# Performance work log

Hardware: AMD Instinct MI355X
Metric: run time of the kernel (lower is better)

## Reference

```python
import jax, jax.numpy as jnp
import numpy as np
from jax.ops import segment_sum

N_NODES = 100000
N_EDGES = 3200000
N_GRAPHS = 64


def gcn_conv(x, W, b, src, dst, n_nodes):
    # Linear transform first (PyG GCNConv applies lin before propagate)
    h = x @ W  # [N, out]
    # Add self loops
    loop = jnp.arange(n_nodes, dtype=src.dtype)
    s = jnp.concatenate([src, loop])
    d = jnp.concatenate([dst, loop])
    # Symmetric normalization deg^-1/2 (deg counts incoming edges incl. self loop)
    deg = segment_sum(jnp.ones_like(d, dtype=h.dtype), d, num_segments=n_nodes)
    dinv = jnp.where(deg > 0, jax.lax.rsqrt(deg), 0.0)
    norm = dinv[s] * dinv[d]  # [E+N]
    # Gather messages from source, scale, scatter-add to target
    msg = h[s] * norm[:, None]
    out = segment_sum(msg, d, num_segments=n_nodes)
    return out + b


def setup_inputs() -> dict:
    key = jax.random.key(0)
    ks = jax.random.split(key, 6)
    x = jax.random.normal(ks[0], (N_NODES, 128), dtype=jnp.float32)
    edge_index = jax.random.randint(ks[1], (2, N_EDGES), 0, N_NODES, dtype=jnp.int64)
    batch = jnp.sort(jax.random.randint(ks[2], (N_NODES,), 0, N_GRAPHS, dtype=jnp.int64))
    W1 = jax.random.normal(ks[3], (128, 256), dtype=jnp.float32) * (1.0 / np.sqrt(128))
    b1 = jnp.zeros((256,), dtype=jnp.float32)
    W2 = jax.random.normal(ks[4], (256, 128), dtype=jnp.float32) * (1.0 / np.sqrt(256))
    b2 = jnp.zeros((128,), dtype=jnp.float32)
    return {"x": x, "edge_index": edge_index, "batch": batch,
            "W1": W1, "b1": b1, "W2": W2, "b2": b2, "num_graphs": N_GRAPHS}


def reference(x, edge_index, batch, W1, b1, W2, b2, num_graphs):
    n_nodes = x.shape[0]
    src, dst = edge_index[0], edge_index[1]
    # dropout(p=0.6, training=False) is identity at inference
    h = jax.nn.relu(gcn_conv(x, W1, b1, src, dst, n_nodes))
    h = gcn_conv(h, W2, b2, src, dst, n_nodes)
    # global_mean_pool by graph id
    sums = segment_sum(h, batch, num_segments=num_graphs)
    counts = segment_sum(jnp.ones((n_nodes,), dtype=h.dtype), batch, num_segments=num_graphs)
    return sums / jnp.maximum(counts, 1.0)[:, None]
```

## Files before the change

### kernel.cpp

```cpp
#include <hip/hip_runtime.h>
#include <hip/hip_bf16.h>
#include <stdint.h>

#define N_NODES 100000
#define N_EDGES 3200000
#define N_GRAPHS 64
#define BSH 8
#define NB 391
#define G_SC 512
#define EPB 6250

typedef unsigned int u32;
typedef unsigned short u16;
typedef __attribute__((ext_vector_type(8))) short bf16x8;
typedef __attribute__((ext_vector_type(4))) float f32x4;

__device__ __forceinline__ float bf_lo(u32 u){ return __uint_as_float(u << 16); }
__device__ __forceinline__ float bf_hi(u32 u){ return __uint_as_float(u & 0xffff0000u); }
__device__ __forceinline__ u16 f2bf(float f){
    union { __hip_bfloat16 h; u16 u; } c; c.h = __float2bfloat16(f); return c.u;
}
__device__ __forceinline__ u32 pack2(float a, float b){
    return (u32)f2bf(a) | ((u32)f2bf(b) << 16);
}

__global__ __launch_bounds__(512) void k_hist(const int* __restrict__ dst,
                                              int* __restrict__ hist){
    __shared__ int h[NB];
    int tid = threadIdx.x, g = blockIdx.x;
    for (int i = tid; i < NB; i += 512) h[i] = 0;
    __syncthreads();
    const int2* d2 = reinterpret_cast<const int2*>(dst + g * EPB);
    for (int i = tid; i < EPB / 2; i += 512){
        int2 d = d2[i];
        atomicAdd(&h[d.x >> BSH], 1);
        atomicAdd(&h[d.y >> BSH], 1);
    }
    __syncthreads();
    for (int i = tid; i < NB; i += 512) hist[i * G_SC + g] = h[i];
}

__global__ __launch_bounds__(512) void k_colscan(const int* __restrict__ hist,
                                                 int* __restrict__ cursors,
                                                 int* __restrict__ btot){
    __shared__ int sm[512];
    int b = blockIdx.x, tid = threadIdx.x;
    int v = hist[b * G_SC + tid];
    sm[tid] = v; __syncthreads();
    for (int off = 1; off < 512; off <<= 1){
        int t = (tid >= off) ? sm[tid - off] : 0;
        __syncthreads(); sm[tid] += t; __syncthreads();
    }
    cursors[b * G_SC + tid] = sm[tid] - v;
    if (tid == 511) btot[b] = sm[511];
}

__global__ __launch_bounds__(512) void k_bscan(const int* __restrict__ btot,
                                               int* __restrict__ bbase){
    __shared__ int sm[512];
    int tid = threadIdx.x;
    int v = (tid < NB) ? btot[tid] : 0;
    sm[tid] = v; __syncthreads();
    for (int off = 1; off < 512; off <<= 1){
        int t = (tid >= off) ? sm[tid - off] : 0;
        __syncthreads(); sm[tid] += t; __syncthreads();
    }
    if (tid < NB) bbase[tid] = sm[tid] - v;
    if (tid == 0) bbase[NB] = N_EDGES;
}

__global__ __launch_bounds__(512) void k_scatter(const int* __restrict__ src,
                                                 const int* __restrict__ dst,
                                                 const int* __restrict__ cursors,
                                                 const int* __restrict__ bbase,
                                                 uint2* __restrict__ pairs){
    __shared__ int cur[NB];
    int g = blockIdx.x, tid = threadIdx.x;
    for (int i = tid; i < NB; i += 512) cur[i] = cursors[i * G_SC + g] + bbase[i];
    __syncthreads();
    const int2* s2 = reinterpret_cast<const int2*>(src + g * EPB);
    const int2* d2 = reinterpret_cast<const int2*>(dst + g * EPB);
    for (int i = tid; i < EPB / 2; i += 512){
        int2 s = s2[i]; int2 d = d2[i];
        int p0 = atomicAdd(&cur[d.x >> BSH], 1);
        pairs[p0] = make_uint2((u32)s.x, (u32)d.x);
        int p1 = atomicAdd(&cur[d.y >> BSH], 1);
        pairs[p1] = make_uint2((u32)s.y, (u32)d.y);
    }
}

__global__ __launch_bounds__(512) void k_fine(const uint2* __restrict__ pairs,
                                              const int* __restrict__ bbase,
                                              int* __restrict__ offsets,
                                              float* __restrict__ dinv,
                                              int* __restrict__ csr_src){
    __shared__ int ldeg[256];
    __shared__ int ssc[256];
    __shared__ int lcur[256];
    int b = blockIdx.x, tid = threadIdx.x;
    int node0 = b << BSH;
    if (tid < 256) ldeg[tid] = 0;
    __syncthreads();
    int e0 = bbase[b], e1 = bbase[b + 1];
    for (int e = e0 + tid; e < e1; e += 512)
        atomicAdd(&ldeg[pairs[e].y - node0], 1);
    __syncthreads();
    int myDeg = (tid < 256) ? ldeg[tid] : 0;
    if (tid < 256) ssc[tid] = myDeg;
    __syncthreads();
    for (int off = 1; off < 256; off <<= 1){
        int t = 0;
        if (tid >= off && tid < 256) t = ssc[tid - off];
        __syncthreads();
        if (tid < 256) ssc[tid] += t;
        __syncthreads();
    }
    if (tid < 256){
        int excl = ssc[tid] - myDeg;
        int n = node0 + tid;
        if (n <= N_NODES) offsets[n] = e0 + excl;
        if (n < N_NODES)  dinv[n] = rsqrtf((float)myDeg + 1.0f);
        lcur[tid] = e0 + excl;
    }
    __syncthreads();
    for (int e = e0 + tid; e < e1; e += 512){
        uint2 p = pairs[e];
        int pos = atomicAdd(&lcur[p.y - node0], 1);
        csr_src[pos] = (int)p.x;
    }
}

__global__ void k_cvt_x(const float* __restrict__ x, const float* __restrict__ dinv,
                        u32* __restrict__ xb){
    int i = blockIdx.x * blockDim.x + threadIdx.x;
    if (i < N_NODES * 32){
        float w = dinv[i >> 5];
        float4 f = reinterpret_cast<const float4*>(x)[i];
        uint2 p = make_uint2(pack2(f.x * w, f.y * w), pack2(f.z * w, f.w * w));
        reinterpret_cast<uint2*>(xb)[i] = p;
    }
}

__global__ void k_cvt_w(const float* __restrict__ W1, const float* __restrict__ W2,
                        u16* __restrict__ w1t, u16* __restrict__ w2t){
    int i = blockIdx.x * blockDim.x + threadIdx.x;
    if (i < 128 * 256){
        int n = i / 128, k = i % 128;
        w1t[i] = f2bf(W1[k * 256 + n]);
    } else {
        int j = i - 128 * 256;
        int n = j / 256, k = j % 256;
        w2t[j] = f2bf(W2[k * 128 + n]);
    }
}

template<bool OUT_BF16>
__global__ __launch_bounds__(256) void k_agg(const u32* __restrict__ X,
                      const int* __restrict__ offs, const int* __restrict__ csr_src,
                      const float* __restrict__ dinv, void* __restrict__ out){
    int lane = threadIdx.x & 63;
    int v = blockIdx.x * 4 + (threadIdx.x >> 6);
    u32 u = X[v * 64 + lane];
    float a0 = bf_lo(u), a1 = bf_hi(u);
    int e1 = offs[v + 1];
    for (int e = offs[v]; e < e1; e += 64){
        int idx = e + lane;
        int sv = (idx < e1) ? csr_src[idx] : 0;
        int cnt = min(64, e1 - e);
        int j = 0;
        for (; j + 4 <= cnt; j += 4){
            int s0 = __shfl(sv, j), s1 = __shfl(sv, j+1), s2 = __shfl(sv, j+2), s3 = __shfl(sv, j+3);
            u32 u0 = X[s0*64 + lane], u1 = X[s1*64 + lane], u2 = X[s2*64 + lane], u3 = X[s3*64 + lane];
            a0 += (bf_lo(u0) + bf_lo(u1)) + (bf_lo(u2) + bf_lo(u3));
            a1 += (bf_hi(u0) + bf_hi(u1)) + (bf_hi(u2) + bf_hi(u3));
        }
        for (; j < cnt; j++){
            int s = __shfl(sv, j);
            u32 uu = X[s*64 + lane];
            a0 += bf_lo(uu); a1 += bf_hi(uu);
        }
    }
    float w = dinv[v];
    a0 *= w; a1 *= w;
    if (OUT_BF16){
        ((u32*)out)[v*64 + lane] = pack2(a0, a1);
    } else {
        ((float2*)out)[v*64 + lane] = make_float2(a0, a1);
    }
}

template<int BK, int BN, bool RELU, bool BIAS, bool SCALE>
__global__ __launch_bounds__(256) void k_gemm(const u16* __restrict__ A, const u16* __restrict__ BT,
                        const float* __restrict__ bias, const float* __restrict__ rowscale,
                        u16* __restrict__ C, int M){
    extern __shared__ char smem[];
    char* As = smem;
    char* Bs = smem + 64 * BK * 2;
    const int tid = threadIdx.x;
    const int rowbytes = BK * 2;
    {
        const int a16 = 64 * rowbytes / 16;
        for (int it = tid; it < a16; it += 256){
            int flat = it * 16;
            int r = flat / rowbytes, cb = flat % rowbytes;
            int grow = blockIdx.x * 64 + r;
            int4 val = make_int4(0,0,0,0);
            if (grow < M) val = *reinterpret_cast<const int4*>(A + grow * BK + cb / 2);
            *reinterpret_cast<int4*>(As + r * rowbytes + (cb ^ ((r & 7) << 4))) = val;
        }
        const int b16 = BN * rowbytes / 16;
        for (int it = tid; it < b16; it += 256){
            int flat = it * 16;
            int r = flat / rowbytes, cb = flat % rowbytes;
            int4 val = *reinterpret_cast<const int4*>(BT + r * BK + cb / 2);
            *reinterpret_cast<int4*>(Bs + r * rowbytes + (cb ^ ((r & 7) << 4))) = val;
        }
    }
    __syncthreads();

    const int wid = tid >> 6, lane = tid & 63;
    const int r0 = wid * 16;
    constexpr int NF = BN / 16;
    f32x4 acc[NF];
#pragma unroll
    for (int i = 0; i < NF; i++) acc[i] = (f32x4){0.f,0.f,0.f,0.f};
    const int ar = r0 + (lane & 15);
    const int koff = (lane >> 4) * 8;
#pragma unroll
    for (int kb = 0; kb < BK / 32; kb++){
        int kbyte = (kb * 32 + koff) * 2;
        bf16x8 aF = *reinterpret_cast<const bf16x8*>(As + ar * rowbytes + (kbyte ^ ((ar & 7) << 4)));
#pragma unroll
        for (int nf = 0; nf < NF; nf++){
            int bn = nf * 16 + (lane & 15);
            bf16x8 bF = *reinterpret_cast<const bf16x8*>(Bs + bn * rowbytes + (kbyte ^ ((bn & 7) << 4)));
            acc[nf] = __builtin_amdgcn_mfma_f32_16x16x32_bf16(aF, bF, acc[nf], 0, 0, 0);
        }
    }
#pragma unroll
    for (int nf = 0; nf < NF; nf++){
        int col = nf * 16 + (lane & 15);
        float bv = BIAS ? bias[col] : 0.f;
#pragma unroll
        for (int j = 0; j < 4; j++){
            int grow = blockIdx.x * 64 + r0 + (lane >> 4) * 4 + j;
            if (grow < M){
                float val = acc[nf][j] + bv;
                if (RELU) val = fmaxf(val, 0.f);
                if (SCALE) val *= rowscale[grow];
                C[grow * BN + col] = f2bf(val);
            }
        }
    }
}

__global__ void k_pool(const float* __restrict__ agg2f, const int* __restrict__ batch,
                       float* __restrict__ psum, float* __restrict__ counts){
    const int NPB = 200;
    int n0 = blockIdx.x * NPB, n1 = min(n0 + NPB, N_NODES);
    int tid = threadIdx.x;
    float racc = 0.f; int gcur = batch[n0]; int runlen = 0;
    for (int n = n0; n < n1; n++){
        int g = batch[n];
        if (g != gcur){
            atomicAdd(&psum[gcur * 128 + tid], racc);
            if (tid == 0) atomicAdd(&counts[gcur], (float)runlen);
            racc = 0.f; runlen = 0; gcur = g;
        }
        racc += agg2f[n * 128 + tid];
        runlen++;
    }
    atomicAdd(&psum[gcur * 128 + tid], racc);
    if (tid == 0) atomicAdd(&counts[gcur], (float)runlen);
}

__global__ void k_final(const float* __restrict__ psum, const float* __restrict__ counts,
                        const float* __restrict__ b2, float* __restrict__ out){
    int g = blockIdx.x, c = threadIdx.x;
    out[g * 128 + c] = psum[g * 128 + c] / fmaxf(counts[g], 1.0f) + b2[c];
}

extern "C" void kernel_launch(void* const* d_in, const int* in_sizes, int n_in,
                              void* d_out, int out_size, void* d_ws, size_t ws_size,
                              hipStream_t stream){
    const float* x   = (const float*)d_in[0];
    const int*   ei  = (const int*)d_in[1];
    const int* batch = (const int*)d_in[2];
    const float* W1  = (const float*)d_in[3];
    const float* b1  = (const float*)d_in[4];
    const float* W2  = (const float*)d_in[5];
    const float* b2  = (const float*)d_in[6];
    float* out = (float*)d_out;
    const int* esrc = ei;
    const int* edst = ei + N_EDGES;

    char* w = (char*)d_ws;
    size_t off = 0;
    auto alloc = [&](size_t bytes) -> char* {
        char* p = w + off; off += (bytes + 255) & ~size_t(255); return p;
    };
    float* dinv     = (float*)alloc((size_t)N_NODES * 4);
    int*   offsets  = (int*)  alloc((size_t)(N_NODES + 1) * 4);
    int*   hist     = (int*)  alloc((size_t)NB * G_SC * 4);
    int*   cursors  = (int*)  alloc((size_t)NB * G_SC * 4);
    int*   btot     = (int*)  alloc((size_t)NB * 4);
    int*   bbase    = (int*)  alloc((size_t)(NB + 1) * 4);
    int*   csr_src  = (int*)  alloc((size_t)N_EDGES * 4);
    u32*   xb       = (u32*)  alloc((size_t)N_NODES * 64 * 4);
    u16*   aggx     = (u16*)  alloc((size_t)N_NODES * 128 * 2);
    u16*   h        = (u16*)  alloc((size_t)N_NODES * 256 * 2);
    u16*   t        = (u16*)  alloc((size_t)N_NODES * 128 * 2);
    u16*   w1t      = (u16*)  alloc(128 * 256 * 2);
    u16*   w2t      = (u16*)  alloc(256 * 128 * 2);
    float* psum     = (float*)alloc((size_t)N_GRAPHS * 128 * 4);
    float* counts   = (float*)alloc((size_t)N_GRAPHS * 4);
    float* agg2f    = (float*)h;
    uint2* pairs    = (uint2*)h;

    hipMemsetAsync(psum, 0, (size_t)N_GRAPHS * 128 * 4, stream);
    hipMemsetAsync(counts, 0, (size_t)N_GRAPHS * 4, stream);

    k_hist   <<<G_SC, 512, 0, stream>>>(edst, hist);
    k_colscan<<<NB, 512, 0, stream>>>(hist, cursors, btot);
    k_bscan  <<<1, 512, 0, stream>>>(btot, bbase);
    k_scatter<<<G_SC, 512, 0, stream>>>(esrc, edst, cursors, bbase, pairs);
    k_fine   <<<NB, 512, 0, stream>>>(pairs, bbase, offsets, dinv, csr_src);

    k_cvt_x<<<12500, 256, 0, stream>>>(x, dinv, xb);
    k_cvt_w<<<256, 256, 0, stream>>>(W1, W2, w1t, w2t);

    k_agg<true><<<25000, 256, 0, stream>>>(xb, offsets, csr_src, dinv, aggx);

    hipFuncSetAttribute(reinterpret_cast<const void*>(&k_gemm<128, 256, true, true, false>),
                        hipFuncAttributeMaxDynamicSharedMemorySize, 64*128*2 + 256*128*2);
    hipFuncSetAttribute(reinterpret_cast<const void*>(&k_gemm<256, 128, false, false, true>),
                        hipFuncAttributeMaxDynamicSharedMemorySize, 64*256*2 + 128*256*2);

    k_gemm<128, 256, true, true, false><<<1563, 256, 64*128*2 + 256*128*2, stream>>>(
        aggx, w1t, b1, nullptr, h, N_NODES);
    k_gemm<256, 128, false, false, true><<<1563, 256, 64*256*2 + 128*256*2, stream>>>(
        h, w2t, nullptr, dinv, t, N_NODES);
    k_agg<false><<<25000, 256, 0, stream>>>((const u32*)t, offsets, csr_src, dinv, (void*)agg2f);
    k_pool <<<500, 128, 0, stream>>>(agg2f, batch, psum, counts);
    k_final<<<N_GRAPHS, 128, 0, stream>>>(psum, counts, b2, out);
}
```

Baseline: 619.1 us.

## Column-chunk feature layout for cache-local aggregation, packed edge pairs, GEMM B from global

Stores node features in 8 column-chunk tables of 16 bf16 values each, so every aggregation pass over a chunk gathers from a 3.2MB table that can stay cache-resident. The aggregation kernel now runs over a 2D grid with 8 lanes per row and 8 edges in flight, followed by a shuffle reduction. The GEMMs read and write these chunked layouts, and the B operand is read straight from global/L1 instead of being staged in LDS. Edge pairs are packed into one 32-bit word (source plus low 8 bits of destination) to halve scatter traffic. Risks: the CSR index array is re-read once per chunk (8x), and unstaged B loads may slow the GEMM.

Measured after the change: 968.4 us. 1.56x slower.

```diff
diff --git a/kernel.cpp b/kernel.cpp
--- a/kernel.cpp
+++ b/kernel.cpp
@@ -73,7 +73,7 @@
                                                  const int* __restrict__ dst,
                                                  const int* __restrict__ cursors,
                                                  const int* __restrict__ bbase,
-                                                 uint2* __restrict__ pairs){
+                                                 u32* __restrict__ pairs){
     __shared__ int cur[NB];
     int g = blockIdx.x, tid = threadIdx.x;
     for (int i = tid; i < NB; i += 512) cur[i] = cursors[i * G_SC + g] + bbase[i];
@@ -83,13 +83,13 @@
     for (int i = tid; i < EPB / 2; i += 512){
         int2 s = s2[i]; int2 d = d2[i];
         int p0 = atomicAdd(&cur[d.x >> BSH], 1);
-        pairs[p0] = make_uint2((u32)s.x, (u32)d.x);
+        pairs[p0] = (u32)s.x | ((u32)(d.x & 255) << 24);
         int p1 = atomicAdd(&cur[d.y >> BSH], 1);
-        pairs[p1] = make_uint2((u32)s.y, (u32)d.y);
-    }
-}
-
-__global__ __launch_bounds__(512) void k_fine(const uint2* __restrict__ pairs,
+        pairs[p1] = (u32)s.y | ((u32)(d.y & 255) << 24);
+    }
+}
+
+__global__ __launch_bounds__(512) void k_fine(const u32* __restrict__ pairs,
                                               const int* __restrict__ bbase,
                                               int* __restrict__ offsets,
                                               float* __restrict__ dinv,
@@ -103,7 +103,7 @@
     __syncthreads();
     int e0 = bbase[b], e1 = bbase[b + 1];
     for (int e = e0 + tid; e < e1; e += 512)
-        atomicAdd(&ldeg[pairs[e].y - node0], 1);
+        atomicAdd(&ldeg[pairs[e] >> 24], 1);
     __syncthreads();
     int myDeg = (tid < 256) ? ldeg[tid] : 0;
     if (tid < 256) ssc[tid] = myDeg;
@@ -124,20 +124,22 @@
     }
     __syncthreads();
     for (int e = e0 + tid; e < e1; e += 512){
-        uint2 p = pairs[e];
-        int pos = atomicAdd(&lcur[p.y - node0], 1);
-        csr_src[pos] = (int)p.x;
+        u32 p = pairs[e];
+        int pos = atomicAdd(&lcur[p >> 24], 1);
+        csr_src[pos] = (int)(p & 0xFFFFFFu);
     }
 }
 
 __global__ void k_cvt_x(const float* __restrict__ x, const float* __restrict__ dinv,
-                        u32* __restrict__ xb){
+                        u32* __restrict__ XC){
     int i = blockIdx.x * blockDim.x + threadIdx.x;
     if (i < N_NODES * 32){
-        float w = dinv[i >> 5];
+        int n = i >> 5, q = i & 31;
+        float w = dinv[n];
         float4 f = reinterpret_cast<const float4*>(x)[i];
         uint2 p = make_uint2(pack2(f.x * w, f.y * w), pack2(f.z * w, f.w * w));
-        reinterpret_cast<uint2*>(xb)[i] = p;
+        int c = q >> 2, r = q & 3;
+        reinterpret_cast<uint2*>(XC)[((size_t)c * N_NODES + n) * 4 + r] = p;
     }
 }
 
@@ -155,65 +157,74 @@
 }
 
 template<bool OUT_BF16>
-__global__ __launch_bounds__(256) void k_agg(const u32* __restrict__ X,
+__global__ __launch_bounds__(256) void k_aggc(const u32* __restrict__ XC,
                       const int* __restrict__ offs, const int* __restrict__ csr_src,
                       const float* __restrict__ dinv, void* __restrict__ out){
     int lane = threadIdx.x & 63;
     int v = blockIdx.x * 4 + (threadIdx.x >> 6);
-    u32 u = X[v * 64 + lane];
-    float a0 = bf_lo(u), a1 = bf_hi(u);
-    int e1 = offs[v + 1];
-    for (int e = offs[v]; e < e1; e += 64){
-        int idx = e + lane;
-        int sv = (idx < e1) ? csr_src[idx] : 0;
-        int cnt = min(64, e1 - e);
-        int j = 0;
-        for (; j + 4 <= cnt; j += 4){
-            int s0 = __shfl(sv, j), s1 = __shfl(sv, j+1), s2 = __shfl(sv, j+2), s3 = __shfl(sv, j+3);
-            u32 u0 = X[s0*64 + lane], u1 = X[s1*64 + lane], u2 = X[s2*64 + lane], u3 = X[s3*64 + lane];
-            a0 += (bf_lo(u0) + bf_lo(u1)) + (bf_lo(u2) + bf_lo(u3));
-            a1 += (bf_hi(u0) + bf_hi(u1)) + (bf_hi(u2) + bf_hi(u3));
-        }
-        for (; j < cnt; j++){
-            int s = __shfl(sv, j);
-            u32 uu = X[s*64 + lane];
-            a0 += bf_lo(uu); a1 += bf_hi(uu);
-        }
-    }
+    int c = blockIdx.y;
+    const u32* tbl = XC + (size_t)c * N_NODES * 8;
+    int sub = lane & 7;
+    int g   = lane >> 3;
+    float a0 = 0.f, a1 = 0.f;
+    int e0 = offs[v], e1 = offs[v + 1];
+    int base = e0;
+    for (; base + 16 <= e1; base += 16){
+        int s0 = csr_src[base + g];
+        int s1 = csr_src[base + 8 + g];
+        u32 u0 = tbl[s0 * 8 + sub];
+        u32 u1 = tbl[s1 * 8 + sub];
+        a0 += bf_lo(u0) + bf_lo(u1);
+        a1 += bf_hi(u0) + bf_hi(u1);
+    }
+    for (; base < e1; base += 8){
+        int e = base + g;
+        if (e < e1){
+            int s = csr_src[e];
+            u32 u = tbl[s * 8 + sub];
+            a0 += bf_lo(u); a1 += bf_hi(u);
+        }
+    }
+    a0 += __shfl_xor(a0, 8);  a1 += __shfl_xor(a1, 8);
+    a0 += __shfl_xor(a0, 16); a1 += __shfl_xor(a1, 16);
+    a0 += __shfl_xor(a0, 32); a1 += __shfl_xor(a1, 32);
+    u32 us = tbl[v * 8 + sub];
     float w = dinv[v];
-    a0 *= w; a1 *= w;
-    if (OUT_BF16){
-        ((u32*)out)[v*64 + lane] = pack2(a0, a1);
-    } else {
-        ((float2*)out)[v*64 + lane] = make_float2(a0, a1);
-    }
-}
-
-template<int BK, int BN, bool RELU, bool BIAS, bool SCALE>
+    a0 = (a0 + bf_lo(us)) * w;
+    a1 = (a1 + bf_hi(us)) * w;
+    if (lane < 8){
+        size_t idx = ((size_t)c * N_NODES + v) * 8 + lane;
+        if (OUT_BF16) ((u32*)out)[idx] = pack2(a0, a1);
+        else          ((float2*)out)[idx] = make_float2(a0, a1);
+    }
+}
+
+template<int BK, int BN, bool RELU, bool BIAS, bool SCALE, bool CHUNKA, bool CHUNKC>
 __global__ __launch_bounds__(256) void k_gemm(const u16* __restrict__ A, const u16* __restrict__ BT,
                         const float* __restrict__ bias, const float* __restrict__ rowscale,
                         u16* __restrict__ C, int M){
-    extern __shared__ char smem[];
-    char* As = smem;
-    char* Bs = smem + 64 * BK * 2;
+    __shared__ char As[64 * BK * 2];
     const int tid = threadIdx.x;
     const int rowbytes = BK * 2;
-    {
-        const int a16 = 64 * rowbytes / 16;
-        for (int it = tid; it < a16; it += 256){
+    const int units = 8 * BK;
+    if (CHUNKA){
+        for (int it = tid; it < units; it += 256){
+            int chunk = it >> 7, rem = it & 127;
+            int r = rem >> 1, half = rem & 1;
+            int grow = blockIdx.x * 64 + r;
+            int4 val = make_int4(0,0,0,0);
+            if (grow < M) val = *reinterpret_cast<const int4*>(A + ((size_t)chunk * M + grow) * 16 + half * 8);
+            int cb = chunk * 32 + half * 16;
+            *reinterpret_cast<int4*>(As + r * rowbytes + (cb ^ ((r & 7) << 4))) = val;
+        }
+    } else {
+        for (int it = tid; it < units; it += 256){
             int flat = it * 16;
             int r = flat / rowbytes, cb = flat % rowbytes;
             int grow = blockIdx.x * 64 + r;
             int4 val = make_int4(0,0,0,0);
-            if (grow < M) val = *reinterpret_cast<const int4*>(A + grow * BK + cb / 2);
+            if (grow < M) val = *reinterpret_cast<const int4*>(A + (size_t)grow * BK + cb / 2);
             *reinterpret_cast<int4*>(As + r * rowbytes + (cb ^ ((r & 7) << 4))) = val;
-        }
-        const int b16 = BN * rowbytes / 16;
-        for (int it = tid; it < b16; it += 256){
-            int flat = it * 16;
-            int r = flat / rowbytes, cb = flat % rowbytes;
-            int4 val = *reinterpret_cast<const int4*>(BT + r * BK + cb / 2);
-            *reinterpret_cast<int4*>(Bs + r * rowbytes + (cb ^ ((r & 7) << 4))) = val;
         }
     }
     __syncthreads();
@@ -233,7 +244,7 @@
 #pragma unroll
         for (int nf = 0; nf < NF; nf++){
             int bn = nf * 16 + (lane & 15);
-            bf16x8 bF = *reinterpret_cast<const bf16x8*>(Bs + bn * rowbytes + (kbyte ^ ((bn & 7) << 4)));
+            bf16x8 bF = *reinterpret_cast<const bf16x8*>(BT + bn * BK + kb * 32 + koff);
             acc[nf] = __builtin_amdgcn_mfma_f32_16x16x32_bf16(aF, bF, acc[nf], 0, 0, 0);
         }
     }
@@ -248,17 +259,20 @@
                 float val = acc[nf][j] + bv;
                 if (RELU) val = fmaxf(val, 0.f);
                 if (SCALE) val *= rowscale[grow];
-                C[grow * BN + col] = f2bf(val);
+                size_t idx = CHUNKC ? ((size_t)(col >> 4) * M + grow) * 16 + (col & 15)
+                                    : (size_t)grow * BN + col;
+                C[idx] = f2bf(val);
             }
         }
     }
 }
 
-__global__ void k_pool(const float* __restrict__ agg2f, const int* __restrict__ batch,
+__global__ void k_pool(const float* __restrict__ agg2fC, const int* __restrict__ batch,
                        float* __restrict__ psum, float* __restrict__ counts){
-    const int NPB = 200;
+    const int NPB = 100;
     int n0 = blockIdx.x * NPB, n1 = min(n0 + NPB, N_NODES);
     int tid = threadIdx.x;
+    size_t choff = (size_t)(tid >> 4) * N_NODES * 16 + (tid & 15);
     float racc = 0.f; int gcur = batch[n0]; int runlen = 0;
     for (int n = n0; n < n1; n++){
         int g = batch[n];
@@ -267,7 +281,7 @@
             if (tid == 0) atomicAdd(&counts[gcur], (float)runlen);
             racc = 0.f; runlen = 0; gcur = g;
         }
-        racc += agg2f[n * 128 + tid];
+        racc += agg2fC[choff + (size_t)n * 16];
         runlen++;
     }
     atomicAdd(&psum[gcur * 128 + tid], racc);
@@ -306,16 +320,16 @@
     int*   btot     = (int*)  alloc((size_t)NB * 4);
     int*   bbase    = (int*)  alloc((size_t)(NB + 1) * 4);
     int*   csr_src  = (int*)  alloc((size_t)N_EDGES * 4);
-    u32*   xb       = (u32*)  alloc((size_t)N_NODES * 64 * 4);
-    u16*   aggx     = (u16*)  alloc((size_t)N_NODES * 128 * 2);
+    u32*   xC       = (u32*)  alloc((size_t)N_NODES * 64 * 4);
+    u16*   aggxC    = (u16*)  alloc((size_t)N_NODES * 128 * 2);
     u16*   h        = (u16*)  alloc((size_t)N_NODES * 256 * 2);
-    u16*   t        = (u16*)  alloc((size_t)N_NODES * 128 * 2);
+    u16*   tC       = (u16*)  alloc((size_t)N_NODES * 128 * 2);
     u16*   w1t      = (u16*)  alloc(128 * 256 * 2);
     u16*   w2t      = (u16*)  alloc(256 * 128 * 2);
     float* psum     = (float*)alloc((size_t)N_GRAPHS * 128 * 4);
     float* counts   = (float*)alloc((size_t)N_GRAPHS * 4);
-    float* agg2f    = (float*)h;
-    uint2* pairs    = (uint2*)h;
+    float* agg2fC   = (float*)h;
+    u32*   pairs    = (u32*)h;
 
     hipMemsetAsync(psum, 0, (size_t)N_GRAPHS * 128 * 4, stream);
     hipMemsetAsync(counts, 0, (size_t)N_GRAPHS * 4, stream);
@@ -326,21 +340,15 @@
     k_scatter<<<G_SC, 512, 0, stream>>>(esrc, edst, cursors, bbase, pairs);
     k_fine   <<<NB, 512, 0, stream>>>(pairs, bbase, offsets, dinv, csr_src);
 
-    k_cvt_x<<<12500, 256, 0, stream>>>(x, dinv, xb);
+    k_cvt_x<<<12500, 256, 0, stream>>>(x, dinv, xC);
     k_cvt_w<<<256, 256, 0, stream>>>(W1, W2, w1t, w2t);
 
-    k_agg<true><<<25000, 256, 0, stream>>>(xb, offsets, csr_src, dinv, aggx);
-
-    hipFuncSetAttribute(reinterpret_cast<const void*>(&k_gemm<128, 256, true, true, false>),
-                        hipFuncAttributeMaxDynamicSharedMemorySize, 64*128*2 + 256*128*2);
-    hipFuncSetAttribute(reinterpret_cast<const void*>(&k_gemm<256, 128, false, false, true>),
-                        hipFuncAttributeMaxDynamicSharedMemorySize, 64*256*2 + 128*256*2);
-
-    k_gemm<128, 256, true, true, false><<<1563, 256, 64*128*2 + 256*128*2, stream>>>(
-        aggx, w1t, b1, nullptr, h, N_NODES);
-    k_gemm<256, 128, false, false, true><<<1563, 256, 64*256*2 + 128*256*2, stream>>>(
-        h, w2t, nullptr, dinv, t, N_NODES);
-    k_agg<false><<<25000, 256, 0, stream>>>((const u32*)t, offsets, csr_src, dinv, (void*)agg2f);
-    k_pool <<<500, 128, 0, stream>>>(agg2f, batch, psum, counts);
+    k_aggc<true><<<dim3(25000, 8), 256, 0, stream>>>(xC, offsets, csr_src, dinv, aggxC);
+    k_gemm<128, 256, true, true, false, true, false><<<1563, 256, 0, stream>>>(
+        aggxC, w1t, b1, nullptr, h, N_NODES);
+    k_gemm<256, 128, false, false, true, false, true><<<1563, 256, 0, stream>>>(
+        h, w2t, nullptr, dinv, tC, N_NODES);
+    k_aggc<false><<<dim3(25000, 8), 256, 0, stream>>>((const u32*)tC, offsets, csr_src, dinv, (void*)agg2fC);
+    k_pool <<<1000, 128, 0, stream>>>(agg2fC, batch, psum, counts);
     k_final<<<N_GRAPHS, 128, 0, stream>>>(psum, counts, b2, out);
 }
```
